# Kernel optimization log

Measured on AMD Instinct MI355X. Metric: run time of the kernel, lower is better.

The kernel has to match this reference:

```python
import jax, jax.numpy as jnp
import numpy as np

ALPHA = 0.8  # LeakyReLU negative slope (nn.LeakyReLU(self.alpha))
OUT_DIM = 64
EDGE_DIM = 32


def setup_inputs() -> dict:
    key = jax.random.key(0)
    ks = jax.random.split(key, 6)
    N, S, IN_D = 50000, 16, 128
    xav = lambda k, shp: jax.random.uniform(k, shp, jnp.float32, -1.0, 1.0) * (1.414 * np.sqrt(6.0 / (shp[0] + shp[1])))
    return {
        "input": jax.random.normal(ks[0], (N, IN_D), jnp.float32),
        "neigh_feat": jax.random.normal(ks[1], (N * S, IN_D), jnp.float32),
        "edge_emb": jax.random.normal(ks[2], (N * S, EDGE_DIM), jnp.float32),
        "W": xav(ks[3], (IN_D, OUT_DIM)),
        "W2": xav(ks[4], (IN_D, OUT_DIM)),
        "a": xav(ks[5], (2 * OUT_DIM + EDGE_DIM, 1)),
    }


def reference(input, neigh_feat, edge_emb, W, W2, a):
    N = input.shape[0]
    S = neigh_feat.shape[0] // N
    D = W.shape[1]
    E = edge_emb.shape[1]

    x = input @ W                               # [N, D]
    neighs = (neigh_feat @ W2).reshape(N, S, D)  # [N, S, D]
    ee = edge_emb.reshape(N, S, E)               # [N, S, E]

    # a_input = cat([x_rep, neighs, ee], -1); e = leakyrelu(a_input @ a)
    # Split a to avoid materializing the concatenated [N, S, 2D+E] tensor.
    a_x, a_n, a_e = a[:D, 0], a[D:2 * D, 0], a[2 * D:, 0]
    scores = (x @ a_x)[:, None] + neighs @ a_n + ee @ a_e   # [N, S]
    e = jnp.where(scores > 0, scores, ALPHA * scores)        # LeakyReLU

    attention = jax.nn.softmax(e, axis=1)        # softmax over neighbors
    # dropout is a no-op in eval mode (training=False)

    h_prime = jnp.einsum("ns,nsd->nd", attention, neighs)    # [N, D]
    h_edge = jnp.einsum("ns,nse->ne", attention, ee)         # [N, E]

    # concat_node=True, concat_edge=True, activation=None
    return jnp.concatenate([x, h_prime, h_edge], axis=1)      # [N, 2D+E]
```

## Files before the change

### kernel.cpp

```cpp
#include <hip/hip_runtime.h>
#include <hip/hip_fp16.h>


#define BAR() do {                                              \
    asm volatile("s_waitcnt lgkmcnt(0)" ::: "memory");          \
    __builtin_amdgcn_s_barrier();                               \
    asm volatile("" ::: "memory");                               \
} while (0)

#define GLDS16(gp, lp) __builtin_amdgcn_global_load_lds(                     \
    (const __attribute__((address_space(1))) void*)(gp),                     \
    (__attribute__((address_space(3))) void*)(lp), 16, 0, 0)
#define GLDS4(gp, lp)  __builtin_amdgcn_global_load_lds(                     \
    (const __attribute__((address_space(1))) void*)(gp),                     \
    (__attribute__((address_space(3))) void*)(lp), 4, 0, 0)

__device__ __forceinline__ float dot4(float4 a, float4 b) {
    return fmaf(a.x, b.x, fmaf(a.y, b.y, fmaf(a.z, b.z, a.w * b.w)));
}

__global__ __launch_bounds__(256)
void prep_kernel(const float* __restrict__ W,
                 const float* __restrict__ W2,
                 const float* __restrict__ a,
                 float* __restrict__ ws) {
    const int t = threadIdx.x;
    __shared__ float s_a[160];
    if (t < 160) { float v = a[t]; s_a[t] = v; ws[128 + t] = v; }
    __syncthreads();
    if (t < 128) {
        float p = 0.f, pw = 0.f;
        #pragma unroll
        for (int d = 0; d < 64; d++) {
            p  = fmaf(W2[t * 64 + d], s_a[64 + d], p);
            pw = fmaf(W [t * 64 + d], s_a[d],      pw);
        }
        ws[t] = p;
        ws[288 + t] = pw;
    }
}

__device__ __forceinline__ void dma_node(const float* __restrict__ neigh,
                                         const float* __restrict__ edge,
                                         const float* __restrict__ input,
                                         int node, int lane,
                                         float* ng, float* ee, float* inb) {
    const float* gn = neigh + (size_t)node * 2048;
    #pragma unroll
    for (int i = 0; i < 8; i++) GLDS16(gn + i * 256 + lane * 4, ng + i * 256);
    const float* ge = edge + (size_t)node * 512;
    #pragma unroll
    for (int i = 0; i < 2; i++) GLDS16(ge + i * 256 + lane * 4, ee + i * 256);
    const float* gi = input + (size_t)node * 128;
    #pragma unroll
    for (int i = 0; i < 2; i++) GLDS4(gi + i * 64 + lane, inb + i * 64);
}

__global__ __launch_bounds__(256, 3)
void gat_attn(const float* __restrict__ input,
              const float* __restrict__ neigh,
              const float* __restrict__ edge,
              const float* __restrict__ ws,
              float* __restrict__ out, int N) {
    const int t = threadIdx.x;
    const int q = t >> 6;
    const int lane = t & 63;

    __shared__ __align__(16) float s_w2a[128];
    __shared__ __align__(16) float s_wa[128];
    __shared__ __align__(16) float s_ae[32];
    __shared__ __align__(16) float s_ng[2][2][2048];
    __shared__ __align__(16) float s_ee[2][2][512];
    __shared__ __align__(16) float s_in[2][2][128];
    __shared__ __align__(16) float s_sc[32];
    __shared__ float s_sx[2];

    if (t < 128) { s_w2a[t] = ws[t]; s_wa[t] = ws[288 + t]; }
    else if (t < 160) s_ae[t - 128] = ws[128 + t];

    const int P = (N + 1) >> 1;
    const int stride = gridDim.x;
    int p = blockIdx.x;
    int cur = 0;

    if (q == 3 && p < P) {
        dma_node(neigh, edge, input, 2 * p, lane,
                 s_ng[0][0], s_ee[0][0], s_in[0][0]);
        dma_node(neigh, edge, input, min(2 * p + 1, N - 1), lane,
                 s_ng[0][1], s_ee[0][1], s_in[0][1]);
        asm volatile("s_waitcnt vmcnt(0)" ::: "memory");
    }
    BAR();

    for (; p < P; p += stride, cur ^= 1) {
        const int nA = 2 * p;
        const int nB = min(2 * p + 1, N - 1);
        const int pn = p + stride;

        if (q == 3) {
            if (pn < P) {
                dma_node(neigh, edge, input, 2 * pn, lane,
                         s_ng[cur ^ 1][0], s_ee[cur ^ 1][0], s_in[cur ^ 1][0]);
                dma_node(neigh, edge, input, min(2 * pn + 1, N - 1), lane,
                         s_ng[cur ^ 1][1], s_ee[cur ^ 1][1], s_in[cur ^ 1][1]);
            }
            const float2 ia = ((const float2*)s_in[cur][0])[lane];
            const float2 ib = ((const float2*)s_in[cur][1])[lane];
            const float2 w  = ((const float2*)s_wa)[lane];
            float pa = fmaf(ia.x, w.x, ia.y * w.y);
            float pb = fmaf(ib.x, w.x, ib.y * w.y);
            #pragma unroll
            for (int off = 32; off; off >>= 1) {
                pa += __shfl_xor(pa, off, 64);
                pb += __shfl_xor(pb, off, 64);
            }
            if (lane == 0) { s_sx[0] = pa; s_sx[1] = pb; }
        }

        {
            const int r = t >> 3, g = t & 7;
            const int node = r >> 4, s = r & 15;
            const float4* ng4  = (const float4*)(s_ng[cur][node] + s * 128);
            const float4* w2a4 = (const float4*)s_w2a;
            float pp = dot4(ng4[g],      w2a4[g])
                     + dot4(ng4[g + 8],  w2a4[g + 8])
                     + dot4(ng4[g + 16], w2a4[g + 16])
                     + dot4(ng4[g + 24], w2a4[g + 24]);
            pp += dot4(((const float4*)(s_ee[cur][node] + s * 32))[g],
                       ((const float4*)s_ae)[g]);
            pp += __shfl_down(pp, 4, 8);
            pp += __shfl_down(pp, 2, 8);
            pp += __shfl_down(pp, 1, 8);
            if (g == 0) s_sc[r] = pp;
        }
        BAR();

        {
            const int node = q & 1, half = q >> 1;
            const int n = node ? nB : nA;
            const float sx = s_sx[node];
            float e[16];
            #pragma unroll
            for (int j = 0; j < 4; j++) {
                float4 v = ((const float4*)s_sc)[node * 4 + j];
                v.x += sx; v.y += sx; v.z += sx; v.w += sx;
                e[4*j+0] = v.x > 0.f ? v.x : 0.8f * v.x;
                e[4*j+1] = v.y > 0.f ? v.y : 0.8f * v.y;
                e[4*j+2] = v.z > 0.f ? v.z : 0.8f * v.z;
                e[4*j+3] = v.w > 0.f ? v.w : 0.8f * v.w;
            }
            float m[8];
            #pragma unroll
            for (int i = 0; i < 8; i++) m[i] = fmaxf(e[i], e[i + 8]);
            #pragma unroll
            for (int i = 0; i < 4; i++) m[i] = fmaxf(m[i], m[i + 4]);
            const float mx = fmaxf(fmaxf(m[0], m[2]), fmaxf(m[1], m[3]));
            #pragma unroll
            for (int s = 0; s < 16; s++) e[s] = __expf(e[s] - mx);
            float sm[8];
            #pragma unroll
            for (int i = 0; i < 8; i++) sm[i] = e[i] + e[i + 8];
            #pragma unroll
            for (int i = 0; i < 4; i++) sm[i] = sm[i] + sm[i + 4];
            const float rinv = 1.0f / ((sm[0] + sm[2]) + (sm[1] + sm[3]));

            if (lane < 20) {
                const int fc = half * 20 + lane;
                if (fc < 32) {
                    const float4* col = (const float4*)s_ng[cur][node] + fc;
                    float4 acc = make_float4(0.f, 0.f, 0.f, 0.f);
                    #pragma unroll
                    for (int s = 0; s < 16; s++) {
                        const float4 v = col[s * 32];
                        acc.x = fmaf(e[s], v.x, acc.x);
                        acc.y = fmaf(e[s], v.y, acc.y);
                        acc.z = fmaf(e[s], v.z, acc.z);
                        acc.w = fmaf(e[s], v.w, acc.w);
                    }
                    union { __half2 h[2]; float2 f; } u;
                    u.h[0] = __floats2half2_rn(acc.x * rinv, acc.y * rinv);
                    u.h[1] = __floats2half2_rn(acc.z * rinv, acc.w * rinv);
                    ((float2*)(out + (size_t)n * 160 + 64))[fc] = u.f;
                } else {
                    const int ec = fc - 32;
                    const float4* col = (const float4*)s_ee[cur][node] + ec;
                    float4 acc = make_float4(0.f, 0.f, 0.f, 0.f);
                    #pragma unroll
                    for (int s = 0; s < 16; s++) {
                        const float4 v = col[s * 8];
                        acc.x = fmaf(e[s], v.x, acc.x);
                        acc.y = fmaf(e[s], v.y, acc.y);
                        acc.z = fmaf(e[s], v.z, acc.z);
                        acc.w = fmaf(e[s], v.w, acc.w);
                    }
                    acc.x *= rinv; acc.y *= rinv; acc.z *= rinv; acc.w *= rinv;
                    *(float4*)(out + (size_t)n * 160 + 128 + (ec << 2)) = acc;
                }
            }
        }
        if (q == 3) asm volatile("s_waitcnt vmcnt(0)" ::: "memory");
        BAR();
    }
}

__global__ __launch_bounds__(256, 2)
void post_gemm(const float* __restrict__ input,
               const float* __restrict__ W,
               const float* __restrict__ W2,
               float* __restrict__ out, int N) {
    const int t = threadIdx.x;
    const int NB = (N + 63) >> 6;
    const bool second = ((int)blockIdx.x >= NB);
    const int rbase = (second ? blockIdx.x - NB : blockIdx.x) << 6;
    const int nrows = min(64, N - rbase);
    const float* Wsrc = second ? W2 : W;
    const int dstcol = second ? 64 : 0;

    __shared__ __align__(16) float sS[64 * 128];
    __shared__ __align__(16) float sW[128 * 64];

    #pragma unroll
    for (int i = 0; i < 8; i++) {
        const int idx = t + i * 256;
        ((float4*)sW)[idx] = ((const float4*)Wsrc)[idx];
    }
    if (!second) {
        #pragma unroll
        for (int i = 0; i < 8; i++) {
            const int idx = t + i * 256;
            const int r = idx >> 5;
            float4 v = make_float4(0.f, 0.f, 0.f, 0.f);
            if (r < nrows)
                v = ((const float4*)(input + (size_t)(rbase + r) * 128))[idx & 31];
            ((float4*)sS)[idx] = v;
        }
    } else {
        #pragma unroll
        for (int i = 0; i < 8; i++) {
            const int idx = t + i * 256;
            const int r = idx >> 5, j = idx & 31;
            float4 v = make_float4(0.f, 0.f, 0.f, 0.f);
            if (r < nrows) {
                union { float2 f; __half2 h[2]; } u;
                u.f = ((const float2*)(out + (size_t)(rbase + r) * 160 + 64))[j];
                const float2 lo = __half22float2(u.h[0]);
                const float2 hi = __half22float2(u.h[1]);
                v = make_float4(lo.x, lo.y, hi.x, hi.y);
            }
            ((float4*)sS)[idx] = v;
        }
    }
    __syncthreads();

    const int r0 = ((t >> 4) & 15) << 2, c0 = (t & 15) << 2;
    float4 acc0 = make_float4(0,0,0,0), acc1 = acc0, acc2 = acc0, acc3 = acc0;
    #pragma unroll 2
    for (int k4 = 0; k4 < 32; k4++) {
        const int k = k4 << 2;
        const float4 a0 = *(const float4*)(sS + (r0 + 0) * 128 + k);
        const float4 a1 = *(const float4*)(sS + (r0 + 1) * 128 + k);
        const float4 a2 = *(const float4*)(sS + (r0 + 2) * 128 + k);
        const float4 a3 = *(const float4*)(sS + (r0 + 3) * 128 + k);
        const float4 w0 = *(const float4*)(sW + (k + 0) * 64 + c0);
        const float4 w1 = *(const float4*)(sW + (k + 1) * 64 + c0);
        const float4 w2 = *(const float4*)(sW + (k + 2) * 64 + c0);
        const float4 w3 = *(const float4*)(sW + (k + 3) * 64 + c0);
        #define MADROW(ACC, A)                                              \
            ACC.x = fmaf(A.x, w0.x, ACC.x); ACC.y = fmaf(A.x, w0.y, ACC.y); \
            ACC.z = fmaf(A.x, w0.z, ACC.z); ACC.w = fmaf(A.x, w0.w, ACC.w); \
            ACC.x = fmaf(A.y, w1.x, ACC.x); ACC.y = fmaf(A.y, w1.y, ACC.y); \
            ACC.z = fmaf(A.y, w1.z, ACC.z); ACC.w = fmaf(A.y, w1.w, ACC.w); \
            ACC.x = fmaf(A.z, w2.x, ACC.x); ACC.y = fmaf(A.z, w2.y, ACC.y); \
            ACC.z = fmaf(A.z, w2.z, ACC.z); ACC.w = fmaf(A.z, w2.w, ACC.w); \
            ACC.x = fmaf(A.w, w3.x, ACC.x); ACC.y = fmaf(A.w, w3.y, ACC.y); \
            ACC.z = fmaf(A.w, w3.z, ACC.z); ACC.w = fmaf(A.w, w3.w, ACC.w);
        MADROW(acc0, a0) MADROW(acc1, a1) MADROW(acc2, a2) MADROW(acc3, a3)
        #undef MADROW
    }
    if (r0 + 0 < nrows) *(float4*)(out + (size_t)(rbase + r0 + 0) * 160 + dstcol + c0) = acc0;
    if (r0 + 1 < nrows) *(float4*)(out + (size_t)(rbase + r0 + 1) * 160 + dstcol + c0) = acc1;
    if (r0 + 2 < nrows) *(float4*)(out + (size_t)(rbase + r0 + 2) * 160 + dstcol + c0) = acc2;
    if (r0 + 3 < nrows) *(float4*)(out + (size_t)(rbase + r0 + 3) * 160 + dstcol + c0) = acc3;
}

extern "C" void kernel_launch(void* const* d_in, const int* in_sizes, int n_in,
                              void* d_out, int out_size, void* d_ws, size_t ws_size,
                              hipStream_t stream) {
    const float* input = (const float*)d_in[0];
    const float* neigh = (const float*)d_in[1];
    const float* edge  = (const float*)d_in[2];
    const float* W     = (const float*)d_in[3];
    const float* W2    = (const float*)d_in[4];
    const float* a     = (const float*)d_in[5];
    float* ws = (float*)d_ws;
    float* out = (float*)d_out;

    const int N = in_sizes[0] / 128;
    const int NB = (N + 63) >> 6;

    prep_kernel<<<1, 256, 0, stream>>>(W, W2, a, ws);
    gat_attn<<<768, 256, 0, stream>>>(input, neigh, edge, ws, out, N);
    post_gemm<<<2 * NB, 256, 0, stream>>>(input, W, W2, out, N);
}
```

Before: 661.9 us.

## Triple-buffer LDS prefetch in gat_attn to keep two node pairs in flight

```diff
diff --git a/kernel.cpp b/kernel.cpp
--- a/kernel.cpp
+++ b/kernel.cpp
@@ -56,7 +56,7 @@
     for (int i = 0; i < 2; i++) GLDS4(gi + i * 64 + lane, inb + i * 64);
 }
 
-__global__ __launch_bounds__(256, 3)
+__global__ __launch_bounds__(256, 2)
 void gat_attn(const float* __restrict__ input,
               const float* __restrict__ neigh,
               const float* __restrict__ edge,
@@ -69,9 +69,9 @@
     __shared__ __align__(16) float s_w2a[128];
     __shared__ __align__(16) float s_wa[128];
     __shared__ __align__(16) float s_ae[32];
-    __shared__ __align__(16) float s_ng[2][2][2048];
-    __shared__ __align__(16) float s_ee[2][2][512];
-    __shared__ __align__(16) float s_in[2][2][128];
+    __shared__ __align__(16) float s_ng[3][2][2048];
+    __shared__ __align__(16) float s_ee[3][2][512];
+    __shared__ __align__(16) float s_in[3][2][128];
     __shared__ __align__(16) float s_sc[32];
     __shared__ float s_sx[2];
 
@@ -81,31 +81,35 @@
     const int P = (N + 1) >> 1;
     const int stride = gridDim.x;
     int p = blockIdx.x;
-    int cur = 0;
+    int sl = 0;
 
     if (q == 3 && p < P) {
         dma_node(neigh, edge, input, 2 * p, lane,
                  s_ng[0][0], s_ee[0][0], s_in[0][0]);
         dma_node(neigh, edge, input, min(2 * p + 1, N - 1), lane,
                  s_ng[0][1], s_ee[0][1], s_in[0][1]);
-        asm volatile("s_waitcnt vmcnt(0)" ::: "memory");
+        const int p1 = min(p + stride, P - 1);
+        dma_node(neigh, edge, input, 2 * p1, lane,
+                 s_ng[1][0], s_ee[1][0], s_in[1][0]);
+        dma_node(neigh, edge, input, min(2 * p1 + 1, N - 1), lane,
+                 s_ng[1][1], s_ee[1][1], s_in[1][1]);
+        asm volatile("s_waitcnt vmcnt(24)" ::: "memory");
     }
     BAR();
 
-    for (; p < P; p += stride, cur ^= 1) {
+    for (; p < P; p += stride) {
         const int nA = 2 * p;
         const int nB = min(2 * p + 1, N - 1);
-        const int pn = p + stride;
+        const int s2 = sl < 1 ? sl + 2 : sl - 1;
 
         if (q == 3) {
-            if (pn < P) {
-                dma_node(neigh, edge, input, 2 * pn, lane,
-                         s_ng[cur ^ 1][0], s_ee[cur ^ 1][0], s_in[cur ^ 1][0]);
-                dma_node(neigh, edge, input, min(2 * pn + 1, N - 1), lane,
-                         s_ng[cur ^ 1][1], s_ee[cur ^ 1][1], s_in[cur ^ 1][1]);
-            }
-            const float2 ia = ((const float2*)s_in[cur][0])[lane];
-            const float2 ib = ((const float2*)s_in[cur][1])[lane];
+            const int p2 = min(p + 2 * stride, P - 1);
+            dma_node(neigh, edge, input, 2 * p2, lane,
+                     s_ng[s2][0], s_ee[s2][0], s_in[s2][0]);
+            dma_node(neigh, edge, input, min(2 * p2 + 1, N - 1), lane,
+                     s_ng[s2][1], s_ee[s2][1], s_in[s2][1]);
+            const float2 ia = ((const float2*)s_in[sl][0])[lane];
+            const float2 ib = ((const float2*)s_in[sl][1])[lane];
             const float2 w  = ((const float2*)s_wa)[lane];
             float pa = fmaf(ia.x, w.x, ia.y * w.y);
             float pb = fmaf(ib.x, w.x, ib.y * w.y);
@@ -120,13 +124,13 @@
         {
             const int r = t >> 3, g = t & 7;
             const int node = r >> 4, s = r & 15;
-            const float4* ng4  = (const float4*)(s_ng[cur][node] + s * 128);
+            const float4* ng4  = (const float4*)(s_ng[sl][node] + s * 128);
             const float4* w2a4 = (const float4*)s_w2a;
             float pp = dot4(ng4[g],      w2a4[g])
                      + dot4(ng4[g + 8],  w2a4[g + 8])
                      + dot4(ng4[g + 16], w2a4[g + 16])
                      + dot4(ng4[g + 24], w2a4[g + 24]);
-            pp += dot4(((const float4*)(s_ee[cur][node] + s * 32))[g],
+            pp += dot4(((const float4*)(s_ee[sl][node] + s * 32))[g],
                        ((const float4*)s_ae)[g]);
             pp += __shfl_down(pp, 4, 8);
             pp += __shfl_down(pp, 2, 8);
@@ -167,7 +171,7 @@
             if (lane < 20) {
                 const int fc = half * 20 + lane;
                 if (fc < 32) {
-                    const float4* col = (const float4*)s_ng[cur][node] + fc;
+                    const float4* col = (const float4*)s_ng[sl][node] + fc;
                     float4 acc = make_float4(0.f, 0.f, 0.f, 0.f);
                     #pragma unroll
                     for (int s = 0; s < 16; s++) {
@@ -183,7 +187,7 @@
                     ((float2*)(out + (size_t)n * 160 + 64))[fc] = u.f;
                 } else {
                     const int ec = fc - 32;
-                    const float4* col = (const float4*)s_ee[cur][node] + ec;
+                    const float4* col = (const float4*)s_ee[sl][node] + ec;
                     float4 acc = make_float4(0.f, 0.f, 0.f, 0.f);
                     #pragma unroll
                     for (int s = 0; s < 16; s++) {
@@ -198,8 +202,9 @@
                 }
             }
         }
-        if (q == 3) asm volatile("s_waitcnt vmcnt(0)" ::: "memory");
+        if (q == 3) asm volatile("s_waitcnt vmcnt(24)" ::: "memory");
         BAR();
+        sl = sl < 2 ? sl + 1 : 0;
     }
 }
 
@@ -299,6 +304,6 @@
     const int NB = (N + 63) >> 6;
 
     prep_kernel<<<1, 256, 0, stream>>>(W, W2, a, ws);
-    gat_attn<<<768, 256, 0, stream>>>(input, neigh, edge, ws, out, N);
+    gat_attn<<<512, 256, 0, stream>>>(input, neigh, edge, ws, out, N);
     post_gemm<<<2 * NB, 256, 0, stream>>>(input, W, W2, out, N);
 }
```

Result: slower. 676.6 us (+2.2%).
